# Kernel optimization log

Measured on AMD Instinct MI355X. Metric: run time of the kernel, lower is better.

Reference implementation:

```python
import jax, jax.numpy as jnp
import numpy as np

NEG = 1e12  # matches torch's -(1-mask)*1e12 masking constant


def _rope_pointer(qw, kw, mask2d):
    # qw, kw: [B, L, K, H]; mask2d: [B, L, L] bool
    B, L, K, H = qw.shape
    # sinusoidal position embedding, interleaved [sin0,cos0,sin1,cos1,...]
    inv_freq = jnp.power(jnp.float32(10000.0), -2.0 * jnp.arange(H // 2, dtype=jnp.float32) / H)
    ang = jnp.arange(L, dtype=jnp.float32)[:, None] * inv_freq  # [L, H/2]
    cos_pos = jnp.repeat(jnp.cos(ang), 2, axis=-1)[None, :, None, :]  # [1,L,1,H]
    sin_pos = jnp.repeat(jnp.sin(ang), 2, axis=-1)[None, :, None, :]

    def rot(x):
        x2 = jnp.stack([-x[..., 1::2], x[..., ::2]], axis=-1).reshape(x.shape)
        return x * cos_pos + x2 * sin_pos

    q = rot(qw)
    k = rot(kw)
    logits = jnp.einsum('bmhd,bnhd->bhmn', q, k)  # [B,K,L,L]
    m = mask2d[:, None, :, :].astype(logits.dtype)  # [B,1,L,L] broadcasts over K
    return logits * m - (1.0 - m) * NEG


def setup_inputs() -> dict:
    key = jax.random.key(0)
    ks = jax.random.split(key, 8)
    B, L, H = 16, 256, 1024
    tri_hid = arg_hid = eve_hid = 64
    role_num = 60
    scale = 1.0 / np.sqrt(H)
    inp = {
        'cond_bert_embs': jax.random.normal(ks[0], (B, L, H), jnp.float32),
        'tri_W': jax.random.normal(ks[1], (2 * tri_hid, H), jnp.float32) * scale,
        'tri_b': jax.random.normal(ks[2], (2 * tri_hid,), jnp.float32) * 0.01,
        'arg_W': jax.random.normal(ks[3], (2 * arg_hid, H), jnp.float32) * scale,
        'arg_b': jax.random.normal(ks[4], (2 * arg_hid,), jnp.float32) * 0.01,
        'role_W': jax.random.normal(ks[5], (2 * eve_hid * role_num, H), jnp.float32) * scale,
        'role_b': jax.random.normal(ks[6], (2 * eve_hid * role_num,), jnp.float32) * 0.01,
        'word_mask2d': jnp.ones((B, L, L), dtype=bool),
        'triu_mask2d': jnp.triu(jnp.ones((B, L, L), dtype=bool)),
    }
    return inp


def reference(cond_bert_embs, tri_W, tri_b, arg_W, arg_b, role_W, role_b,
              word_mask2d, triu_mask2d):
    B, L, H = cond_bert_embs.shape
    tri_hid = tri_W.shape[0] // 2
    arg_hid = arg_W.shape[0] // 2
    eve_hid = tri_hid  # eve_hid_size == tri_hid_size here
    role_num = role_W.shape[0] // (2 * eve_hid)

    # trigger pointer: K = 1 head
    tri_reps = (cond_bert_embs @ tri_W.T + tri_b).reshape(B, L, 1, 2 * tri_hid)
    tri_qw, tri_kw = jnp.split(tri_reps, 2, axis=-1)
    tri_logits = _rope_pointer(tri_qw, tri_kw, word_mask2d).transpose(0, 2, 3, 1)  # [B,L,L,1]

    # argument pointer: K = 1 head
    arg_reps = (cond_bert_embs @ arg_W.T + arg_b).reshape(B, L, 1, 2 * arg_hid)
    arg_qw, arg_kw = jnp.split(arg_reps, 2, axis=-1)
    arg_logits = _rope_pointer(arg_qw, arg_kw, word_mask2d).transpose(0, 2, 3, 1)  # [B,L,L,1]

    # role pointer: K = role_num heads, upper-triangular mask
    role_reps = (cond_bert_embs @ role_W.T + role_b).reshape(B, L, role_num, 2 * eve_hid)
    role_qw, role_kw = jnp.split(role_reps, 2, axis=-1)
    role_logits = _rope_pointer(role_qw, role_kw, triu_mask2d).transpose(0, 2, 3, 1)
    role_logits = role_logits.reshape(B, L, L, -1, role_num)  # [B,L,L,1,role_num]

    return (tri_logits, arg_logits, role_logits)
```

## Files before the change

kernel.cpp:

```cpp
#include <hip/hip_runtime.h>
#include <hip/hip_bf16.h>
#include <stdint.h>


typedef __attribute__((ext_vector_type(8)))  short short8;
typedef __attribute__((ext_vector_type(4)))  float f32x4;
typedef __attribute__((ext_vector_type(4)))  uint16_t u16x4;

#define LQ    256
#define HID   1024
#define NH    62
#define HSTR  16384
#define NEGF  (-1000727379968.0f)
#define TA_OFF   1048576ULL
#define ROLE_OFF 2097152ULL

__device__ __forceinline__ uint16_t f2bf(float x) {
  uint32_t u = __builtin_bit_cast(uint32_t, x);
  return (uint16_t)((u + 0x7FFFu + ((u >> 16) & 1u)) >> 16);
}
__device__ __forceinline__ uint16_t f2bf_tr(float x) {
  return (uint16_t)(__builtin_bit_cast(uint32_t, x) >> 16);
}
__device__ __forceinline__ float bf2f(uint16_t b) {
  uint32_t u = ((uint32_t)b) << 16;
  return __builtin_bit_cast(float, u);
}
__device__ __forceinline__ int mask_mode(const void* p) {
  uint32_t w0 = *(const uint32_t*)p;
  if (w0 == 0x01010101u) return 0;
  if (w0 == 1u)          return 1;
  if (w0 == 0x3F803F80u) return 2;
  return 3;
}
__device__ __forceinline__ bool mask_at(const void* p, int mode, size_t idx) {
  if (mode == 0) return ((const uint8_t*)p)[idx] != 0;
  if (mode == 1) return ((const int*)p)[idx] != 0;
  if (mode == 2) return (((const uint16_t*)p)[idx] & 0x7FFFu) != 0;
  return ((const float*)p)[idx] != 0.0f;
}
__device__ __forceinline__ void rope_cs(int pos, float invf, float* s, float* c) {
  float ang = (float)pos * invf;
  __sincosf(ang, s, c);
}
__device__ __forceinline__ float rope_invf(int p) {
  return exp2f(-(float)p * (13.287712379549449f / 32.0f));
}
__device__ __forceinline__ void gload16(const short* g, short* l) {
  __builtin_amdgcn_global_load_lds(
      (const __attribute__((address_space(1))) void*)g,
      (__attribute__((address_space(3))) void*)l, 16, 0, 0);
}
__device__ __forceinline__ int xcd_swizzle(int l, int nwg) {
  int xcd = l & 7, idx = l >> 3;
  int q = nwg >> 3, r = nwg & 7;
  int base = (xcd < r) ? xcd * (q + 1) : r * (q + 1) + (xcd - r) * q;
  return base + idx;
}

#define EGRP 524288
#define WGRP 1015808
__global__ __launch_bounds__(256)
void k_preconv(const float* __restrict__ E,
               const float* __restrict__ triW, const float* __restrict__ argW,
               const float* __restrict__ roleW,
               short* __restrict__ Eb, short* __restrict__ Wb) {
  for (int gid = blockIdx.x * 256 + threadIdx.x; gid < EGRP + WGRP;
       gid += gridDim.x * 256) {
    const float* src;
    short* dst;
    if (gid < EGRP) {
      int row = gid >> 7, col8 = gid & 127;
      src = E + (size_t)row * HID + col8 * 8;
      dst = Eb + (((size_t)(row >> 4)) * 32 + (col8 >> 2)) * 512
               + (row & 15) * 32 + (col8 & 3) * 8;
    } else {
      int g = gid - EGRP;
      int row = g >> 7, col8 = g & 127;
      const float* srow = (row < 128) ? triW + (size_t)row * HID
                        : (row < 256) ? argW + (size_t)(row - 128) * HID
                                      : roleW + (size_t)(row - 256) * HID;
      src = srow + col8 * 8;
      dst = Wb + (((size_t)(row >> 4)) * 32 + (col8 >> 2)) * 512
               + (row & 15) * 32 + (col8 & 3) * 8;
    }
    f32x4 v0 = *reinterpret_cast<const f32x4*>(src);
    f32x4 v1 = *reinterpret_cast<const f32x4*>(src + 4);
    short8 r;
    r[0] = (short)f2bf_tr(v0[0]); r[1] = (short)f2bf_tr(v0[1]);
    r[2] = (short)f2bf_tr(v0[2]); r[3] = (short)f2bf_tr(v0[3]);
    r[4] = (short)f2bf_tr(v1[0]); r[5] = (short)f2bf_tr(v1[1]);
    r[6] = (short)f2bf_tr(v1[2]); r[7] = (short)f2bf_tr(v1[3]);
    *reinterpret_cast<short8*>(dst) = r;
  }
}

__global__ __launch_bounds__(256)
void k_proj_pre(const short* __restrict__ Eb, const short* __restrict__ Wb,
                const float* __restrict__ triB, const float* __restrict__ argB,
                const float* __restrict__ roleB,
                short* __restrict__ qs, short* __restrict__ ks, int b0) {
  const int nwg = 62 * gridDim.y;
  const int nl  = xcd_swizzle(blockIdx.x + 62 * blockIdx.y, nwg);
  const int nb = nl % 62;
  const int mb = nl / 62;
  const int n0 = nb * 128;
  const int mrow0 = b0 * LQ + mb * 128;
  const int lrow0 = mb * 128;

  const float* Bv;
  if (nb == 0)      Bv = triB;
  else if (nb == 1) Bv = argB;
  else              Bv = roleB + (n0 - 256);

  __shared__ short As[2][128 * 32];
  __shared__ short Bs[2][128 * 32];

  const int tid  = threadIdx.x;
  const int lane = tid & 63;
  const int w    = tid >> 6;
  const int wm   = (w >> 1) * 64, wn = (w & 1) * 64;
  const int l8   = lane * 8;
  const int mt0  = mrow0 >> 4;
  const int nt0  = n0 >> 4;

  f32x4 acc[4][4] = {};

  auto stage = [&](int buf, int kt) {
#pragma unroll
    for (int cc = 0; cc < 2; ++cc) {
      const int c = w * 2 + cc;
      gload16(Eb + ((size_t)(mt0 + c) * 32 + kt) * 512 + l8, &As[buf][c * 512]);
      gload16(Wb + ((size_t)(nt0 + c) * 32 + kt) * 512 + l8, &Bs[buf][c * 512]);
    }
  };

  stage(0, 0);
  __syncthreads();
  for (int t = 0; t < 32; ++t) {
    const int buf = t & 1;
    if (t + 1 < 32) stage(buf ^ 1, t + 1);
    short8 af[4], bfr[4];
#pragma unroll
    for (int i = 0; i < 4; ++i)
      af[i] = *reinterpret_cast<const short8*>(
          &As[buf][(wm + i * 16 + (lane & 15)) * 32 + (lane >> 4) * 8]);
#pragma unroll
    for (int j = 0; j < 4; ++j)
      bfr[j] = *reinterpret_cast<const short8*>(
          &Bs[buf][(wn + j * 16 + (lane & 15)) * 32 + (lane >> 4) * 8]);
#pragma unroll
    for (int i = 0; i < 4; ++i)
#pragma unroll
      for (int j = 0; j < 4; ++j)
        acc[i][j] = __builtin_amdgcn_mfma_f32_16x16x32_bf16(af[i], bfr[j], acc[i][j], 0, 0, 0);
    __syncthreads();
  }

  const int col_l = lane & 15;
  const int row_h = (lane >> 4) * 4;
#pragma unroll
  for (int j = 0; j < 4; ++j) {
    const int n_loc = wn + j * 16 + col_l;
    const int gcol  = n0 + n_loc;
    const float bias = Bv[n_loc];
    const int d    = gcol & 63;
    const int head = gcol >> 7;
    const bool is_k = (gcol >> 6) & 1;
    const bool odd = d & 1;
    const float invf = rope_invf(d >> 1);
    short* dst = is_k ? ks : qs;
#pragma unroll
    for (int i = 0; i < 4; ++i) {
#pragma unroll
      for (int r = 0; r < 4; ++r) {
        float v  = acc[i][j][r] + bias;
        float vp = __shfl_xor(v, 1, 64);
        int tl  = lrow0 + wm + i * 16 + row_h + r;
        int pos = tl & (LQ - 1);
        float s, c;
        rope_cs(pos, invf, &s, &c);
        float o = odd ? (v * c + vp * s) : (v * c - vp * s);
        dst[((size_t)(tl >> 8) * NH + head) * HSTR + (size_t)pos * 64 + d] =
            (short)f2bf(o);
      }
    }
  }
}

__global__ __launch_bounds__(256)
void k_proj_chunk(const float* __restrict__ E,
                  const float* __restrict__ triW, const float* __restrict__ triB,
                  const float* __restrict__ argW, const float* __restrict__ argB,
                  const float* __restrict__ roleW, const float* __restrict__ roleB,
                  short* __restrict__ qs, short* __restrict__ ks, int b0) {
  const int nb = blockIdx.x;
  const int mb = blockIdx.y;
  const int n0 = nb * 128;
  const int mrow0 = b0 * LQ + mb * 128;
  const int lrow0 = mb * 128;

  const float* W;  const float* Bv;
  if (nb == 0)      { W = triW;                             Bv = triB; }
  else if (nb == 1) { W = argW;                             Bv = argB; }
  else              { W = roleW + (size_t)(n0 - 256) * HID; Bv = roleB + (n0 - 256); }

  __shared__ short As[2][128 * 32];
  __shared__ short Bs[2][128 * 32];

  const int tid  = threadIdx.x;
  const int lane = tid & 63;
  const int w    = tid >> 6;
  const int wm   = (w >> 1) * 64, wn = (w & 1) * 64;
  const int srow = tid >> 2;
  const int scol = (tid & 3) * 8;

  f32x4 acc[4][4] = {};
  f32x4 ra0[2], ra1[2], rb0[2], rb1[2];

  auto load_regs = [&](int k0) {
    const float* pa0 = E + (size_t)(mrow0 + srow) * HID + k0 + scol;
    const float* pa1 = E + (size_t)(mrow0 + 64 + srow) * HID + k0 + scol;
    const float* pb0 = W + (size_t)(srow) * HID + k0 + scol;
    const float* pb1 = W + (size_t)(64 + srow) * HID + k0 + scol;
    ra0[0] = *reinterpret_cast<const f32x4*>(pa0);
    ra0[1] = *reinterpret_cast<const f32x4*>(pa0 + 4);
    ra1[0] = *reinterpret_cast<const f32x4*>(pa1);
    ra1[1] = *reinterpret_cast<const f32x4*>(pa1 + 4);
    rb0[0] = *reinterpret_cast<const f32x4*>(pb0);
    rb0[1] = *reinterpret_cast<const f32x4*>(pb0 + 4);
    rb1[0] = *reinterpret_cast<const f32x4*>(pb1);
    rb1[1] = *reinterpret_cast<const f32x4*>(pb1 + 4);
  };
  auto cvt8 = [&](const f32x4* v) -> short8 {
    short8 r;
    r[0] = (short)f2bf_tr(v[0][0]); r[1] = (short)f2bf_tr(v[0][1]);
    r[2] = (short)f2bf_tr(v[0][2]); r[3] = (short)f2bf_tr(v[0][3]);
    r[4] = (short)f2bf_tr(v[1][0]); r[5] = (short)f2bf_tr(v[1][1]);
    r[6] = (short)f2bf_tr(v[1][2]); r[7] = (short)f2bf_tr(v[1][3]);
    return r;
  };
  auto write_lds = [&](int buf) {
    *reinterpret_cast<short8*>(&As[buf][srow * 32 + scol])        = cvt8(ra0);
    *reinterpret_cast<short8*>(&As[buf][(64 + srow) * 32 + scol]) = cvt8(ra1);
    *reinterpret_cast<short8*>(&Bs[buf][srow * 32 + scol])        = cvt8(rb0);
    *reinterpret_cast<short8*>(&Bs[buf][(64 + srow) * 32 + scol]) = cvt8(rb1);
  };

  load_regs(0); write_lds(0); __syncthreads();
  const int NT = HID / 32;
  for (int t = 0; t < NT; ++t) {
    if (t + 1 < NT) load_regs((t + 1) * 32);
    const int buf = t & 1;
    short8 af[4], bfr[4];
#pragma unroll
    for (int i = 0; i < 4; ++i)
      af[i] = *reinterpret_cast<const short8*>(
          &As[buf][(wm + i * 16 + (lane & 15)) * 32 + (lane >> 4) * 8]);
#pragma unroll
    for (int j = 0; j < 4; ++j)
      bfr[j] = *reinterpret_cast<const short8*>(
          &Bs[buf][(wn + j * 16 + (lane & 15)) * 32 + (lane >> 4) * 8]);
#pragma unroll
    for (int i = 0; i < 4; ++i)
#pragma unroll
      for (int j = 0; j < 4; ++j)
        acc[i][j] = __builtin_amdgcn_mfma_f32_16x16x32_bf16(af[i], bfr[j], acc[i][j], 0, 0, 0);
    __syncthreads();
    if (t + 1 < NT) { write_lds((t + 1) & 1); __syncthreads(); }
  }

  const int col_l = lane & 15;
  const int row_h = (lane >> 4) * 4;
#pragma unroll
  for (int j = 0; j < 4; ++j) {
    const int n_loc = wn + j * 16 + col_l;
    const int gcol  = n0 + n_loc;
    const float bias = Bv[n_loc];
    const int d    = gcol & 63;
    const int head = gcol >> 7;
    const bool is_k = (gcol >> 6) & 1;
    const bool odd = d & 1;
    const float invf = rope_invf(d >> 1);
    short* dst = is_k ? ks : qs;
#pragma unroll
    for (int i = 0; i < 4; ++i) {
#pragma unroll
      for (int r = 0; r < 4; ++r) {
        float v  = acc[i][j][r] + bias;
        float vp = __shfl_xor(v, 1, 64);
        int tl  = lrow0 + wm + i * 16 + row_h + r;
        int pos = tl & (LQ - 1);
        float s, c;
        rope_cs(pos, invf, &s, &c);
        float o = odd ? (v * c + vp * s) : (v * c - vp * s);
        dst[((size_t)(tl >> 8) * NH + head) * HSTR + (size_t)pos * 64 + d] =
            (short)f2bf(o);
      }
    }
  }
}

__global__ __launch_bounds__(512)
void k_role3(const short* __restrict__ qs, const short* __restrict__ ks,
             const void* __restrict__ triu_mask, float* __restrict__ out,
             int b0) {
  const int nwg = gridDim.z * 128;
  const int nl  = xcd_swizzle(blockIdx.x + 8 * blockIdx.y + 128 * blockIdx.z,
                              nwg);
  const int bz  = nl >> 7;
  const int rem = nl & 127;
  const int mt  = rem >> 3, nt = rem & 7;
  const int bg = b0 + bz;
  const int m0 = mt * 16, n0 = nt * 32;
  __shared__ uint16_t tile[16 * 32 * 60];

  const int tid = threadIdx.x, lane = tid & 63, w = tid >> 6;
  const int frow = lane & 15;
  const int koff = (lane >> 4) * 8;
  const size_t cbase = (size_t)bz * NH;

  auto do_head = [&](int r) {
    const size_t hb = (cbase + 2 + r) * HSTR;
    short8 aq[2], bk[2][2];
#pragma unroll
    for (int kc = 0; kc < 2; ++kc) {
      aq[kc] = *reinterpret_cast<const short8*>(
          qs + hb + (size_t)(m0 + frow) * 64 + kc * 32 + koff);
      bk[0][kc] = *reinterpret_cast<const short8*>(
          ks + hb + (size_t)(n0 + frow) * 64 + kc * 32 + koff);
      bk[1][kc] = *reinterpret_cast<const short8*>(
          ks + hb + (size_t)(n0 + 16 + frow) * 64 + kc * 32 + koff);
    }
    f32x4 acc[2] = {};
#pragma unroll
    for (int jf = 0; jf < 2; ++jf)
#pragma unroll
      for (int kc = 0; kc < 2; ++kc)
        acc[jf] = __builtin_amdgcn_mfma_f32_16x16x32_bf16(aq[kc], bk[jf][kc], acc[jf], 0, 0, 0);
#pragma unroll
    for (int jf = 0; jf < 2; ++jf)
#pragma unroll
      for (int rg = 0; rg < 4; ++rg) {
        int m = (lane >> 4) * 4 + rg;
        int n = jf * 16 + (lane & 15);
        tile[(m * 32 + n) * 60 + r] = f2bf(acc[jf][rg]);
      }
  };

  if (w < 4) {
    const int h0 = w * 8;
#pragma unroll 2
    for (int i = 0; i < 8; ++i) do_head(h0 + i);
  } else {
    const int h0 = 32 + (w - 4) * 7;
#pragma unroll 2
    for (int i = 0; i < 7; ++i) do_head(h0 + i);
  }
  __syncthreads();

  const int mode = mask_mode(triu_mask);
  const size_t maskbase = ((size_t)bg * LQ + m0) * LQ + n0;
  const size_t outbase  = ROLE_OFF + (((size_t)bg * LQ + m0) * LQ + n0) * 60;
  for (int f = tid; f < 7680; f += 512) {
    int e  = f * 4;
    int m  = e / 1920;
    int x  = e - m * 1920;
    int n_ = x / 60;
    u16x4 tv = *reinterpret_cast<const u16x4*>(&tile[e]);
    bool mk = mask_at(triu_mask, mode, maskbase + (size_t)m * LQ + n_);
    f32x4 v;
    v[0] = mk ? bf2f(tv[0]) : NEGF;
    v[1] = mk ? bf2f(tv[1]) : NEGF;
    v[2] = mk ? bf2f(tv[2]) : NEGF;
    v[3] = mk ? bf2f(tv[3]) : NEGF;
    *reinterpret_cast<f32x4*>(&out[outbase + (size_t)m * (LQ * 60) + x]) = v;
  }
}

__global__ __launch_bounds__(256)
void k_ta_chunk(const short* __restrict__ qs, const short* __restrict__ ks,
                const void* __restrict__ word_mask, float* __restrict__ out,
                int b0) {
  const int mt = blockIdx.x, h = blockIdx.y, bz = blockIdx.z;
  const int bg = b0 + bz;
  const int m0 = mt * 32;
  __shared__ uint16_t tile[32 * 256];

  const int tid = threadIdx.x, lane = tid & 63, w = tid >> 6;
  const int frow = lane & 31;
  const int koff = (lane >> 5) * 8;
  const size_t hb = ((size_t)bz * NH + h) * HSTR;

  short8 aq[4];
#pragma unroll
  for (int kc = 0; kc < 4; ++kc)
    aq[kc] = *reinterpret_cast<const short8*>(
        qs + hb + (size_t)(m0 + frow) * 64 + kc * 16 + koff);

  typedef __attribute__((ext_vector_type(16))) float f32x16l;
#pragma unroll
  for (int jn = 0; jn < 2; ++jn) {
    const int ncol0 = w * 64 + jn * 32;
    short8 bk[4];
#pragma unroll
    for (int kc = 0; kc < 4; ++kc)
      bk[kc] = *reinterpret_cast<const short8*>(
          ks + hb + (size_t)(ncol0 + frow) * 64 + kc * 16 + koff);
    f32x16l acc = {};
#pragma unroll
    for (int kc = 0; kc < 4; ++kc)
      acc = __builtin_amdgcn_mfma_f32_32x32x16_bf16(aq[kc], bk[kc], acc, 0, 0, 0);
#pragma unroll
    for (int rg = 0; rg < 16; ++rg) {
      int m = (rg & 3) + 8 * (rg >> 2) + 4 * (lane >> 5);
      int n = ncol0 + (lane & 31);
      tile[m * 256 + n] = f2bf(acc[rg]);
    }
  }
  __syncthreads();

  const int mode = mask_mode(word_mask);
  const size_t maskbase = ((size_t)bg * LQ + m0) * LQ;
  const size_t outbase  = (size_t)h * TA_OFF + ((size_t)bg * LQ + m0) * LQ;
  for (int e = tid; e < 8192; e += 256) {
    int m = e >> 8, n = e & 255;
    bool mk = mask_at(word_mask, mode, maskbase + (size_t)m * LQ + n);
    out[outbase + e] = mk ? bf2f(tile[e]) : NEGF;
  }
}

__global__ __launch_bounds__(256)
void k_ta_fused(const float* __restrict__ E,
                const float* __restrict__ triW, const float* __restrict__ triB,
                const float* __restrict__ argW, const float* __restrict__ argB,
                const void* __restrict__ word_mask, float* __restrict__ out) {
  const int h = blockIdx.x, b = blockIdx.y;
  const float* W  = h ? argW : triW;
  const float* Bv = h ? argB : triB;

  __shared__ short As[2][128 * 32];
  __shared__ short Bs[2][128 * 32];
  __shared__ short qk[256 * 128];

  const int tid  = threadIdx.x;
  const int lane = tid & 63;
  const int w    = tid >> 6;
  const int wm   = (w >> 1) * 64, wn = (w & 1) * 64;
  const int srow = tid >> 2;
  const int scol = (tid & 3) * 8;
  const int col_l = lane & 15;
  const int row_h = (lane >> 4) * 4;

  for (int mi = 0; mi < 2; ++mi) {
    const int r0 = mi * 128;
    f32x4 acc[4][4] = {};
    f32x4 ra0[2], ra1[2], rb0[2], rb1[2];
    auto load_regs = [&](int k0) {
      const float* pa0 = E + ((size_t)b * LQ + r0 + srow) * HID + k0 + scol;
      const float* pa1 = E + ((size_t)b * LQ + r0 + 64 + srow) * HID + k0 + scol;
      const float* pb0 = W + (size_t)(srow) * HID + k0 + scol;
      const float* pb1 = W + (size_t)(64 + srow) * HID + k0 + scol;
      ra0[0] = *reinterpret_cast<const f32x4*>(pa0);
      ra0[1] = *reinterpret_cast<const f32x4*>(pa0 + 4);
      ra1[0] = *reinterpret_cast<const f32x4*>(pa1);
      ra1[1] = *reinterpret_cast<const f32x4*>(pa1 + 4);
      rb0[0] = *reinterpret_cast<const f32x4*>(pb0);
      rb0[1] = *reinterpret_cast<const f32x4*>(pb0 + 4);
      rb1[0] = *reinterpret_cast<const f32x4*>(pb1);
      rb1[1] = *reinterpret_cast<const f32x4*>(pb1 + 4);
    };
    auto cvt8 = [&](const f32x4* v) -> short8 {
      short8 r;
      r[0] = (short)f2bf_tr(v[0][0]); r[1] = (short)f2bf_tr(v[0][1]);
      r[2] = (short)f2bf_tr(v[0][2]); r[3] = (short)f2bf_tr(v[0][3]);
      r[4] = (short)f2bf_tr(v[1][0]); r[5] = (short)f2bf_tr(v[1][1]);
      r[6] = (short)f2bf_tr(v[1][2]); r[7] = (short)f2bf_tr(v[1][3]);
      return r;
    };
    auto write_lds = [&](int buf) {
      *reinterpret_cast<short8*>(&As[buf][srow * 32 + scol])        = cvt8(ra0);
      *reinterpret_cast<short8*>(&As[buf][(64 + srow) * 32 + scol]) = cvt8(ra1);
      *reinterpret_cast<short8*>(&Bs[buf][srow * 32 + scol])        = cvt8(rb0);
      *reinterpret_cast<short8*>(&Bs[buf][(64 + srow) * 32 + scol]) = cvt8(rb1);
    };
    load_regs(0); write_lds(0); __syncthreads();
    for (int t = 0; t < 32; ++t) {
      if (t + 1 < 32) load_regs((t + 1) * 32);
      const int buf = t & 1;
      short8 af[4], bfr[4];
#pragma unroll
      for (int i = 0; i < 4; ++i)
        af[i] = *reinterpret_cast<const short8*>(
            &As[buf][(wm + i * 16 + col_l) * 32 + (lane >> 4) * 8]);
#pragma unroll
      for (int j = 0; j < 4; ++j)
        bfr[j] = *reinterpret_cast<const short8*>(
            &Bs[buf][(wn + j * 16 + col_l) * 32 + (lane >> 4) * 8]);
#pragma unroll
      for (int i = 0; i < 4; ++i)
#pragma unroll
        for (int j = 0; j < 4; ++j)
          acc[i][j] = __builtin_amdgcn_mfma_f32_16x16x32_bf16(af[i], bfr[j], acc[i][j], 0, 0, 0);
      __syncthreads();
      if (t + 1 < 32) { write_lds((t + 1) & 1); __syncthreads(); }
    }
#pragma unroll
    for (int j = 0; j < 4; ++j) {
      const int n_loc = wn + j * 16 + col_l;
      const float bias = Bv[n_loc];
      const int d = n_loc & 63;
      const bool odd = d & 1;
      const float invf = rope_invf(d >> 1);
#pragma unroll
      for (int i = 0; i < 4; ++i) {
#pragma unroll
        for (int r = 0; r < 4; ++r) {
          float v  = acc[i][j][r] + bias;
          float vp = __shfl_xor(v, 1, 64);
          int pos = r0 + wm + i * 16 + row_h + r;
          float s, c;
          rope_cs(pos, invf, &s, &c);
          float o = odd ? (v * c + vp * s) : (v * c - vp * s);
          qk[pos * 128 + n_loc] = (short)f2bf(o);
        }
      }
    }
    __syncthreads();
  }

  const int mode = mask_mode(word_mask);
  short8 aq[4][2];
#pragma unroll
  for (int i = 0; i < 4; ++i)
#pragma unroll
    for (int kk = 0; kk < 2; ++kk)
      aq[i][kk] = *reinterpret_cast<const short8*>(
          &qk[(w * 64 + i * 16 + col_l) * 128 + kk * 32 + (lane >> 4) * 8]);

  for (int ncb = 0; ncb < 4; ++ncb) {
    const int nbase = ncb * 64;
    short8 bk[4][2];
#pragma unroll
    for (int j = 0; j < 4; ++j)
#pragma unroll
      for (int kk = 0; kk < 2; ++kk)
        bk[j][kk] = *reinterpret_cast<const short8*>(
            &qk[(nbase + j * 16 + col_l) * 128 + 64 + kk * 32 + (lane >> 4) * 8]);
    f32x4 acc[4][4] = {};
#pragma unroll
    for (int i = 0; i < 4; ++i)
#pragma unroll
      for (int j = 0; j < 4; ++j)
#pragma unroll
        for (int kk = 0; kk < 2; ++kk)
          acc[i][j] = __builtin_amdgcn_mfma_f32_16x16x32_bf16(aq[i][kk], bk[j][kk], acc[i][j], 0, 0, 0);
#pragma unroll
    for (int i = 0; i < 4; ++i)
#pragma unroll
      for (int j = 0; j < 4; ++j)
#pragma unroll
        for (int r = 0; r < 4; ++r) {
          int gm = w * 64 + i * 16 + row_h + r;
          int gn = nbase + j * 16 + col_l;
          size_t mi_ = ((size_t)b * LQ + gm) * LQ + gn;
          bool mk = mask_at(word_mask, mode, mi_);
          out[(size_t)h * TA_OFF + mi_] = mk ? acc[i][j][r] : NEGF;
        }
  }
}

extern "C" void kernel_launch(void* const* d_in, const int* in_sizes, int n_in,
                              void* d_out, int out_size, void* d_ws, size_t ws_size,
                              hipStream_t stream) {
  (void)in_sizes; (void)n_in; (void)out_size;
  const float* E     = (const float*)d_in[0];
  const float* triW  = (const float*)d_in[1];
  const float* triB  = (const float*)d_in[2];
  const float* argW  = (const float*)d_in[3];
  const float* argB  = (const float*)d_in[4];
  const float* roleW = (const float*)d_in[5];
  const float* roleB = (const float*)d_in[6];
  const void*  wmask = d_in[7];
  const void*  tmask = d_in[8];
  float* out = (float*)d_out;

  const size_t PER_B = (size_t)NH * HSTR * 2 * 2;
  const size_t PRE   = ((size_t)4096 * HID + (size_t)7936 * HID) * 2;

  int cb_pre = (ws_size > PRE) ? (int)((ws_size - PRE) / PER_B) : 0;
  if (cb_pre > 16) cb_pre = 16;

  if (cb_pre >= 1) {
    short* qs = (short*)d_ws;
    short* ks = qs + (size_t)cb_pre * NH * HSTR;
    short* Eb = ks + (size_t)cb_pre * NH * HSTR;
    short* Wb = Eb + (size_t)4096 * HID;
    k_preconv<<<dim3(2048), dim3(256), 0, stream>>>(E, triW, argW, roleW, Eb, Wb);
    for (int b0 = 0; b0 < 16; b0 += cb_pre) {
      int cbi = (16 - b0 < cb_pre) ? (16 - b0) : cb_pre;
      k_proj_pre<<<dim3(62, 2 * cbi), dim3(256), 0, stream>>>(
          Eb, Wb, triB, argB, roleB, qs, ks, b0);
      k_role3<<<dim3(8, 16, cbi), dim3(512), 0, stream>>>(qs, ks, tmask, out, b0);
      k_ta_chunk<<<dim3(8, 2, cbi), dim3(256), 0, stream>>>(qs, ks, wmask, out, b0);
    }
    return;
  }

  int cb = (int)(ws_size / PER_B);
  if (cb > 16) cb = 16;
  if (cb >= 1) {
    short* qs = (short*)d_ws;
    short* ks = qs + (size_t)cb * NH * HSTR;
    for (int b0 = 0; b0 < 16; b0 += cb) {
      int cbi = (16 - b0 < cb) ? (16 - b0) : cb;
      k_proj_chunk<<<dim3(62, 2 * cbi), dim3(256), 0, stream>>>(
          E, triW, triB, argW, argB, roleW, roleB, qs, ks, b0);
      k_role3<<<dim3(8, 16, cbi), dim3(512), 0, stream>>>(qs, ks, tmask, out, b0);
      k_ta_chunk<<<dim3(8, 2, cbi), dim3(256), 0, stream>>>(qs, ks, wmask, out, b0);
    }
  } else {
    short* qs = (short*)d_out;
    short* ks = qs + (size_t)NH * HSTR;
    for (int b0 = 0; b0 < 16; ++b0) {
      k_proj_chunk<<<dim3(62, 2), dim3(256), 0, stream>>>(
          E, triW, triB, argW, argB, roleW, roleB, qs, ks, b0);
      k_role3<<<dim3(8, 16, 1), dim3(512), 0, stream>>>(qs, ks, tmask, out, b0);
    }
    k_ta_fused<<<dim3(2, 16), dim3(256), 0, stream>>>(E, triW, triB, argW, argB,
                                                      wmask, out);
  }
}
```

Before: 272.9 us.

## Enlarge role tile to 64 rows and stream heads in groups of twelve

The role-logit kernel now covers a 64x32 output tile per workgroup instead of 16x32, so each K fragment load serves four M-fragments and the grid shrinks fourfold. Heads are processed in five groups of 12 through a smaller shared staging buffer, and each group is flushed to global memory before the next starts. This cuts shared memory per block and improves operand reuse. In exchange, the output writes become 48-byte strided segments per (m,n) instead of contiguous 240-byte runs, it adds extra barriers, and the grid is smaller.

After: 321.8 us. +17.9%, slower.

```diff
diff --git a/kernel.cpp b/kernel.cpp
--- a/kernel.cpp
+++ b/kernel.cpp
@@ -302,79 +302,88 @@
 }
 
 __global__ __launch_bounds__(512)
-void k_role3(const short* __restrict__ qs, const short* __restrict__ ks,
+void k_role5(const short* __restrict__ qs, const short* __restrict__ ks,
              const void* __restrict__ triu_mask, float* __restrict__ out,
              int b0) {
-  const int nwg = gridDim.z * 128;
-  const int nl  = xcd_swizzle(blockIdx.x + 8 * blockIdx.y + 128 * blockIdx.z,
+  const int nwg = gridDim.z * 32;
+  const int nl  = xcd_swizzle(blockIdx.x + 8 * blockIdx.y + 32 * blockIdx.z,
                               nwg);
-  const int bz  = nl >> 7;
-  const int rem = nl & 127;
+  const int bz  = nl >> 5;
+  const int rem = nl & 31;
   const int mt  = rem >> 3, nt = rem & 7;
   const int bg = b0 + bz;
-  const int m0 = mt * 16, n0 = nt * 32;
-  __shared__ uint16_t tile[16 * 32 * 60];
+  const int m0 = mt * 64, n0 = nt * 32;
+  __shared__ uint16_t tile[64 * 32 * 12];
 
   const int tid = threadIdx.x, lane = tid & 63, w = tid >> 6;
+  const int mhalf = w >> 2;
+  const int hslot = w & 3;
   const int frow = lane & 15;
   const int koff = (lane >> 4) * 8;
   const size_t cbase = (size_t)bz * NH;
 
-  auto do_head = [&](int r) {
-    const size_t hb = (cbase + 2 + r) * HSTR;
-    short8 aq[2], bk[2][2];
-#pragma unroll
-    for (int kc = 0; kc < 2; ++kc) {
-      aq[kc] = *reinterpret_cast<const short8*>(
-          qs + hb + (size_t)(m0 + frow) * 64 + kc * 32 + koff);
-      bk[0][kc] = *reinterpret_cast<const short8*>(
-          ks + hb + (size_t)(n0 + frow) * 64 + kc * 32 + koff);
-      bk[1][kc] = *reinterpret_cast<const short8*>(
-          ks + hb + (size_t)(n0 + 16 + frow) * 64 + kc * 32 + koff);
-    }
-    f32x4 acc[2] = {};
-#pragma unroll
-    for (int jf = 0; jf < 2; ++jf)
-#pragma unroll
-      for (int kc = 0; kc < 2; ++kc)
-        acc[jf] = __builtin_amdgcn_mfma_f32_16x16x32_bf16(aq[kc], bk[jf][kc], acc[jf], 0, 0, 0);
-#pragma unroll
-    for (int jf = 0; jf < 2; ++jf)
-#pragma unroll
-      for (int rg = 0; rg < 4; ++rg) {
-        int m = (lane >> 4) * 4 + rg;
-        int n = jf * 16 + (lane & 15);
-        tile[(m * 32 + n) * 60 + r] = f2bf(acc[jf][rg]);
-      }
-  };
-
-  if (w < 4) {
-    const int h0 = w * 8;
-#pragma unroll 2
-    for (int i = 0; i < 8; ++i) do_head(h0 + i);
-  } else {
-    const int h0 = 32 + (w - 4) * 7;
-#pragma unroll 2
-    for (int i = 0; i < 7; ++i) do_head(h0 + i);
-  }
-  __syncthreads();
-
   const int mode = mask_mode(triu_mask);
   const size_t maskbase = ((size_t)bg * LQ + m0) * LQ + n0;
-  const size_t outbase  = ROLE_OFF + (((size_t)bg * LQ + m0) * LQ + n0) * 60;
-  for (int f = tid; f < 7680; f += 512) {
-    int e  = f * 4;
-    int m  = e / 1920;
-    int x  = e - m * 1920;
-    int n_ = x / 60;
-    u16x4 tv = *reinterpret_cast<const u16x4*>(&tile[e]);
-    bool mk = mask_at(triu_mask, mode, maskbase + (size_t)m * LQ + n_);
-    f32x4 v;
-    v[0] = mk ? bf2f(tv[0]) : NEGF;
-    v[1] = mk ? bf2f(tv[1]) : NEGF;
-    v[2] = mk ? bf2f(tv[2]) : NEGF;
-    v[3] = mk ? bf2f(tv[3]) : NEGF;
-    *reinterpret_cast<f32x4*>(&out[outbase + (size_t)m * (LQ * 60) + x]) = v;
+  const size_t outb     = ROLE_OFF + (((size_t)bg * LQ + m0) * LQ + n0) * 60;
+
+  for (int g = 0; g < 5; ++g) {
+#pragma unroll
+    for (int i = 0; i < 3; ++i) {
+      const int rr = hslot * 3 + i;
+      const int r  = g * 12 + rr;
+      const size_t hb = (cbase + 2 + r) * HSTR;
+      short8 aq[2][2], bk[2][2];
+#pragma unroll
+      for (int kc = 0; kc < 2; ++kc) {
+#pragma unroll
+        for (int mf = 0; mf < 2; ++mf)
+          aq[mf][kc] = *reinterpret_cast<const short8*>(
+              qs + hb + (size_t)(m0 + mhalf * 32 + mf * 16 + frow) * 64
+                 + kc * 32 + koff);
+#pragma unroll
+        for (int nf = 0; nf < 2; ++nf)
+          bk[nf][kc] = *reinterpret_cast<const short8*>(
+              ks + hb + (size_t)(n0 + nf * 16 + frow) * 64 + kc * 32 + koff);
+      }
+      f32x4 acc[2][2] = {};
+#pragma unroll
+      for (int mf = 0; mf < 2; ++mf)
+#pragma unroll
+        for (int nf = 0; nf < 2; ++nf)
+#pragma unroll
+          for (int kc = 0; kc < 2; ++kc)
+            acc[mf][nf] = __builtin_amdgcn_mfma_f32_16x16x32_bf16(
+                aq[mf][kc], bk[nf][kc], acc[mf][nf], 0, 0, 0);
+#pragma unroll
+      for (int mf = 0; mf < 2; ++mf)
+#pragma unroll
+        for (int nf = 0; nf < 2; ++nf)
+#pragma unroll
+          for (int rg = 0; rg < 4; ++rg) {
+            int m = mhalf * 32 + mf * 16 + (lane >> 4) * 4 + rg;
+            int n = nf * 16 + (lane & 15);
+            tile[(m * 32 + n) * 12 + rr] = f2bf(acc[mf][nf][rg]);
+          }
+    }
+    __syncthreads();
+
+    for (int f = tid; f < 6144; f += 512) {
+      int e  = f * 4;
+      int m  = e / 384;
+      int x  = e - m * 384;
+      int n_ = x / 12;
+      u16x4 tv = *reinterpret_cast<const u16x4*>(&tile[e]);
+      bool mk = mask_at(triu_mask, mode, maskbase + (size_t)m * LQ + n_);
+      f32x4 v;
+      v[0] = mk ? bf2f(tv[0]) : NEGF;
+      v[1] = mk ? bf2f(tv[1]) : NEGF;
+      v[2] = mk ? bf2f(tv[2]) : NEGF;
+      v[3] = mk ? bf2f(tv[3]) : NEGF;
+      *reinterpret_cast<f32x4*>(
+          &out[outb + (size_t)m * (LQ * 60) + (size_t)n_ * 60 + g * 12
+               + (x - n_ * 12)]) = v;
+    }
+    __syncthreads();
   }
 }
 
@@ -601,7 +610,7 @@
       int cbi = (16 - b0 < cb_pre) ? (16 - b0) : cb_pre;
       k_proj_pre<<<dim3(62, 2 * cbi), dim3(256), 0, stream>>>(
           Eb, Wb, triB, argB, roleB, qs, ks, b0);
-      k_role3<<<dim3(8, 16, cbi), dim3(512), 0, stream>>>(qs, ks, tmask, out, b0);
+      k_role5<<<dim3(8, 4, cbi), dim3(512), 0, stream>>>(qs, ks, tmask, out, b0);
       k_ta_chunk<<<dim3(8, 2, cbi), dim3(256), 0, stream>>>(qs, ks, wmask, out, b0);
     }
     return;
@@ -616,7 +625,7 @@
       int cbi = (16 - b0 < cb) ? (16 - b0) : cb;
       k_proj_chunk<<<dim3(62, 2 * cbi), dim3(256), 0, stream>>>(
           E, triW, triB, argW, argB, roleW, roleB, qs, ks, b0);
-      k_role3<<<dim3(8, 16, cbi), dim3(512), 0, stream>>>(qs, ks, tmask, out, b0);
+      k_role5<<<dim3(8, 4, cbi), dim3(512), 0, stream>>>(qs, ks, tmask, out, b0);
       k_ta_chunk<<<dim3(8, 2, cbi), dim3(256), 0, stream>>>(qs, ks, wmask, out, b0);
     }
   } else {
@@ -625,7 +634,7 @@
     for (int b0 = 0; b0 < 16; ++b0) {
       k_proj_chunk<<<dim3(62, 2), dim3(256), 0, stream>>>(
           E, triW, triB, argW, argB, roleW, roleB, qs, ks, b0);
-      k_role3<<<dim3(8, 16, 1), dim3(512), 0, stream>>>(qs, ks, tmask, out, b0);
+      k_role5<<<dim3(8, 4, 1), dim3(512), 0, stream>>>(qs, ks, tmask, out, b0);
     }
     k_ta_fused<<<dim3(2, 16), dim3(256), 0, stream>>>(E, triW, triB, argW, argB,
                                                       wmask, out);
```
